# Performance work log

Measured on AMD Instinct MI355X. Metric: run time of the kernel, lower is better.

## Reference

```python
import jax, jax.numpy as jnp
import numpy as np

DIM = 192
NUM_HEADS = 6
WH, WW = 7, 7
N = WH * WW  # 49 tokens per window
C2 = 2 * DIM  # concatenated channel dim = 384
SCALE = (DIM // NUM_HEADS) ** -0.5  # module uses dim//num_heads, not C2//num_heads
NW = 64  # number of windows per image
B_ = 2048  # num_windows * batch


def _relative_position_index():
    ch = np.arange(WH)
    cw = np.arange(WW)
    coords = np.stack(np.meshgrid(ch, cw, indexing='ij')).reshape(2, -1)  # [2, N]
    rel = coords[:, :, None] - coords[:, None, :]  # [2, N, N]
    rel = rel.transpose(1, 2, 0).astype(np.int64)  # [N, N, 2]
    rel[..., 0] += WH - 1
    rel[..., 1] += WW - 1
    rel[..., 0] *= 2 * WW - 1
    return jnp.asarray(rel.sum(-1))  # [N, N]

REL_IDX = _relative_position_index()


def setup_inputs() -> dict:
    key = jax.random.key(0)
    ks = jax.random.split(key, 8)
    x = jax.random.normal(ks[0], (B_, N, DIM), dtype=jnp.float32)
    y = jax.random.normal(ks[1], (B_, N, DIM), dtype=jnp.float32)
    mask = jax.random.normal(ks[2], (NW, N, N), dtype=jnp.float32)
    w_qkv = jax.random.normal(ks[3], (6 * DIM, C2), dtype=jnp.float32) * 0.02
    b_qkv = jnp.zeros((6 * DIM,), dtype=jnp.float32)
    w_proj = jax.random.normal(ks[4], (DIM, C2), dtype=jnp.float32) * 0.02
    b_proj = jnp.zeros((DIM,), dtype=jnp.float32)
    bias_table = jax.random.normal(ks[5], ((2 * WH - 1) * (2 * WW - 1), NUM_HEADS), dtype=jnp.float32) * 0.02
    return {"x": x, "y": y, "mask": mask, "w_qkv": w_qkv, "b_qkv": b_qkv,
            "w_proj": w_proj, "b_proj": b_proj, "bias_table": bias_table}


def reference(x, y, mask, w_qkv, b_qkv, w_proj, b_proj, bias_table):
    Bc = x.shape[0]
    Dh = C2 // NUM_HEADS  # 64
    xy = jnp.concatenate([x, y], axis=2)  # [B_, N, 2*dim]
    qkv = xy @ w_qkv.T + b_qkv  # [B_, N, 6*dim]
    qkv = qkv.reshape(Bc, N, 3, NUM_HEADS, Dh).transpose(2, 0, 3, 1, 4)  # [3, B_, H, N, Dh]
    q, k, v = qkv[0] * SCALE, qkv[1], qkv[2]
    attn = jnp.einsum('bhnd,bhmd->bhnm', q, k)  # [B_, H, N, N]
    rpb = bias_table[REL_IDX]  # [N, N, H]
    attn = attn + rpb.transpose(2, 0, 1)[None]
    nW = mask.shape[0]
    attn = attn.reshape(Bc // nW, nW, NUM_HEADS, N, N) + mask[None, :, None]
    attn = attn.reshape(Bc, NUM_HEADS, N, N)
    attn = jax.nn.softmax(attn, axis=-1)
    out = jnp.einsum('bhnm,bhmd->bhnd', attn, v)  # [B_, H, N, Dh]
    out = out.transpose(0, 2, 1, 3).reshape(Bc, N, C2)
    return out @ w_proj.T + b_proj  # [B_, N, dim]
```

## Files before the change

kernel.cpp:

```cpp
#include <hip/hip_runtime.h>
#include <hip/hip_bf16.h>


typedef __attribute__((ext_vector_type(8))) short short8;
typedef __attribute__((ext_vector_type(4))) float f32x4;

#define SCALE 0.17677669529663687f

#define WQF_OFF    0ul
#define WQF_BYTES  (864ul*1024)
#define WPF_OFF    (WQF_OFF + WQF_BYTES)
#define WPF_BYTES  (144ul*1024)
#define COMB_OFF   (WPF_OFF + WPF_BYTES)
#define COMB_BYTES (64ul*6*4096*4)
#define XYF_OFF    (COMB_OFF + COMB_BYTES)
#define XYF_BYTES  (2048ul*48*1024)
#define OF_OFF     (XYF_OFF + XYF_BYTES)
#define OF_BYTES   XYF_BYTES
#define WS_NEED    (OF_OFF + OF_BYTES)

__device__ __forceinline__ unsigned short f2bf(float f){
  unsigned u = __builtin_bit_cast(unsigned, f);
  u = u + 0x7fffu + ((u >> 16) & 1u);
  return (unsigned short)(u >> 16);
}
__device__ __forceinline__ unsigned long long pack4(float4 v){
  return (unsigned long long)f2bf(v.x) | ((unsigned long long)f2bf(v.y) << 16)
       | ((unsigned long long)f2bf(v.z) << 32) | ((unsigned long long)f2bf(v.w) << 48);
}

__global__ void k0_wfrag(const float* __restrict__ wq_f, const float* __restrict__ wp_f,
                         unsigned short* __restrict__ wqf, unsigned short* __restrict__ wpf){
  int t = blockIdx.x*256 + threadIdx.x;
  int fragidx = t >> 6, l = t & 63;
  const float* src; unsigned short* dst;
  if (fragidx < 864){
    int h = fragidx/144, rem = fragidx - h*144;
    int ct = rem/12, kt = rem - ct*12;
    int row = (ct>>2)*384 + h*64 + (ct&3)*16 + (l&15);
    src = wq_f + (long)row*384 + kt*32 + (l>>4)*8;
    dst = wqf + (long)fragidx*512 + l*8;
  } else {
    int fid = fragidx - 864;
    int ct = fid/12, kt = fid - ct*12;
    int row = ct*16 + (l&15);
    src = wp_f + (long)row*384 + kt*32 + (l>>4)*8;
    dst = wpf + (long)fid*512 + l*8;
  }
  short8 v;
  #pragma unroll
  for (int e = 0; e < 8; ++e) v[e] = (short)f2bf(src[e]);
  *(short8*)dst = v;
}

__global__ void prep_comb(const float* __restrict__ mask, const float* __restrict__ btab,
                          float* __restrict__ comb){
  int idx = blockIdx.x * 256 + threadIdx.x;
  int j = idx & 63, i = (idx >> 6) & 63, rest = idx >> 12;
  int h = rest % 6, w = rest / 6;
  float v;
  if (i < 49 && j < 49){
    int di = i / 7 - j / 7 + 6;
    int dj = i % 7 - j % 7 + 6;
    v = btab[(di * 13 + dj) * 6 + h] + mask[(w * 49 + i) * 49 + j];
  } else {
    v = (j >= 49) ? -1e30f : 0.0f;
  }
  comb[idx] = v;
}

__global__ void k1_xyfrag(const float* __restrict__ x, const float* __restrict__ y,
                          unsigned short* __restrict__ xyf){
  const int kt  = blockIdx.x;
  const int win = blockIdx.y;
  const int mt  = threadIdx.x >> 6;
  const int l   = threadIdx.x & 63;
  const int row = mt*16 + (l & 15);
  const int c0  = kt*32 + (l >> 4)*8;
  short8 v = {};
  if (row < 49){
    const float* src = (kt < 6) ? (x + ((long)win*49 + row)*192 + c0)
                                : (y + ((long)win*49 + row)*192 + (c0 - 192));
    float4 f0 = *(const float4*)src, f1 = *(const float4*)(src+4);
    unsigned long long lo = pack4(f0), hi = pack4(f1);
    #pragma unroll
    for (int e = 0; e < 4; ++e){ v[e] = (short)(lo >> (16*e)); v[4+e] = (short)(hi >> (16*e)); }
  }
  *(short8*)(xyf + (((long)win*12 + kt)*4 + mt)*512 + l*8) = v;
}

__device__ __forceinline__ int swz(int r, int b){ return b ^ ((r & 7) << 4); }
__device__ __forceinline__ int a_q (int r, int c){ return 0     + swz(r, r*128 + c*2); }
__device__ __forceinline__ int a_k (int r, int c){ return 8192  + swz(r, r*128 + c*2); }
__device__ __forceinline__ int a_vt(int r, int c){ return 16384 + swz(r, r*128 + c*2); }

__global__ __launch_bounds__(256, 4)
void k2_qkv_attn(const unsigned short* __restrict__ xyf, const unsigned short* __restrict__ wqf,
                 const float* __restrict__ bqkv, const float* __restrict__ comb,
                 unsigned short* __restrict__ Of){
  __shared__ __align__(16) unsigned char smem[24576];
  const int h = blockIdx.x, win = blockIdx.y;
  const int tid = threadIdx.x, w = tid>>6, l = tid&63, l15 = l&15, lg = l>>4;

  float bias[3];
  #pragma unroll
  for (int nt = 0; nt < 3; ++nt){
    int n = w*48 + nt*16 + l15;
    bias[nt] = bqkv[(n>>6)*384 + h*64 + (n&63)];
  }

  f32x4 acc[4][3] = {};
  const unsigned short* Ab = xyf + (long)win*24576;
  const unsigned short* Bb = wqf + ((long)h*12 + w*3)*12*512;
  short8 aA[2][4], bB[2][3];
  #pragma unroll
  for (int mt = 0; mt < 4; ++mt) aA[0][mt] = *(const short8*)(Ab + mt*512 + l*8);
  #pragma unroll
  for (int nt = 0; nt < 3; ++nt) bB[0][nt] = *(const short8*)(Bb + (nt*12)*512 + l*8);
  #pragma unroll
  for (int kt = 0; kt < 12; ++kt){
    const int cur = kt & 1, nxt = cur ^ 1;
    if (kt < 11){
      #pragma unroll
      for (int mt = 0; mt < 4; ++mt)
        aA[nxt][mt] = *(const short8*)(Ab + ((kt+1)*4 + mt)*512 + l*8);
      #pragma unroll
      for (int nt = 0; nt < 3; ++nt)
        bB[nxt][nt] = *(const short8*)(Bb + (nt*12 + kt+1)*512 + l*8);
    }
    #pragma unroll
    for (int nt = 0; nt < 3; ++nt){
      #pragma unroll
      for (int mt = 0; mt < 4; ++mt)
        acc[mt][nt] = __builtin_amdgcn_mfma_f32_16x16x32_bf16(aA[cur][mt], bB[cur][nt], acc[mt][nt], 0, 0, 0);
    }
  }

  const float* cb = comb + ((long)((win & 63)*6 + h))*4096 + (w*16 + l15)*64 + lg*4;
  float4 cbv[4];
  #pragma unroll
  for (int nt = 0; nt < 4; ++nt) cbv[nt] = *(const float4*)(cb + nt*16);

  #pragma unroll
  for (int nt = 0; nt < 3; ++nt){
    int ct = w*3 + nt, s = ct >> 2, d16 = (ct & 3) * 16;
    if (s == 2){
      #pragma unroll
      for (int mt = 0; mt < 4; ++mt){
        float4 vv;
        vv.x = acc[mt][nt][0] + bias[nt]; vv.y = acc[mt][nt][1] + bias[nt];
        vv.z = acc[mt][nt][2] + bias[nt]; vv.w = acc[mt][nt][3] + bias[nt];
        *(unsigned long long*)(smem + a_vt(d16 + l15, mt*16 + lg*4)) = pack4(vv);
      }
    } else {
      float sc = (s == 0) ? SCALE : 1.0f;
      #pragma unroll
      for (int mt = 0; mt < 4; ++mt){
        #pragma unroll
        for (int j = 0; j < 4; ++j){
          int row = mt*16 + lg*4 + j;
          float v = (acc[mt][nt][j] + bias[nt]) * sc;
          int addr = (s == 0) ? a_q(row, d16 + l15) : a_k(row, d16 + l15);
          *(unsigned short*)(smem + addr) = f2bf(v);
        }
      }
    }
  }
  __syncthreads();

  short8 bq[2];
  #pragma unroll
  for (int ks = 0; ks < 2; ++ks)
    bq[ks] = *(const short8*)(smem + a_q(w*16 + l15, ks*32 + lg*8));
  f32x4 st[4] = {};
  #pragma unroll
  for (int ks = 0; ks < 2; ++ks){
    #pragma unroll
    for (int nt = 0; nt < 4; ++nt){
      short8 ak = *(const short8*)(smem + a_k(nt*16 + l15, ks*32 + lg*8));
      st[nt] = __builtin_amdgcn_mfma_f32_16x16x32_bf16(ak, bq[ks], st[nt], 0, 0, 0);
    }
  }
  #pragma unroll
  for (int nt = 0; nt < 4; ++nt){
    st[nt][0] += cbv[nt].x; st[nt][1] += cbv[nt].y;
    st[nt][2] += cbv[nt].z; st[nt][3] += cbv[nt].w;
  }
  float mx;
  {
    float m0 = fmaxf(fmaxf(st[0][0], st[0][1]), fmaxf(st[0][2], st[0][3]));
    float m1 = fmaxf(fmaxf(st[1][0], st[1][1]), fmaxf(st[1][2], st[1][3]));
    float m2 = fmaxf(fmaxf(st[2][0], st[2][1]), fmaxf(st[2][2], st[2][3]));
    float m3 = fmaxf(fmaxf(st[3][0], st[3][1]), fmaxf(st[3][2], st[3][3]));
    mx = fmaxf(fmaxf(m0, m1), fmaxf(m2, m3));
  }
  mx = fmaxf(mx, __shfl_xor(mx, 16));
  mx = fmaxf(mx, __shfl_xor(mx, 32));
  float ssum = 0.f;
  #pragma unroll
  for (int nt = 0; nt < 4; ++nt){
    #pragma unroll
    for (int j = 0; j < 4; ++j){
      float e = __expf(st[nt][j] - mx);
      st[nt][j] = e; ssum += e;
    }
  }
  ssum += __shfl_xor(ssum, 16);
  ssum += __shfl_xor(ssum, 32);
  const float inv = 1.0f / ssum;

  #pragma unroll
  for (int nt = 0; nt < 4; ++nt){
    float4 vv;
    vv.x = st[nt][0]*inv; vv.y = st[nt][1]*inv; vv.z = st[nt][2]*inv; vv.w = st[nt][3]*inv;
    *(unsigned long long*)(smem + a_q(w*16 + l15, nt*16 + lg*4)) = pack4(vv);
  }

  short8 ap[2];
  #pragma unroll
  for (int ks = 0; ks < 2; ++ks)
    ap[ks] = *(const short8*)(smem + a_q(w*16 + l15, ks*32 + lg*8));
  f32x4 oacc[4] = {};
  #pragma unroll
  for (int ks = 0; ks < 2; ++ks){
    #pragma unroll
    for (int nt = 0; nt < 4; ++nt){
      short8 bv = *(const short8*)(smem + a_vt(nt*16 + l15, ks*32 + lg*8));
      oacc[nt] = __builtin_amdgcn_mfma_f32_16x16x32_bf16(ap[ks], bv, oacc[nt], 0, 0, 0);
    }
  }
  #pragma unroll
  for (int nt = 0; nt < 4; ++nt){
    #pragma unroll
    for (int j = 0; j < 4; ++j)
      *(unsigned short*)(smem + a_q(w*16 + lg*4 + j, nt*16 + l15)) = f2bf(oacc[nt][j]);
  }
  unsigned short* Ob = Of + (((long)win*12 + h*2)*4 + w)*512 + l*8;
  #pragma unroll
  for (int ks = 0; ks < 2; ++ks){
    short8 o8 = *(const short8*)(smem + a_q(w*16 + l15, ks*32 + lg*8));
    *(short8*)(Ob + ks*4*512) = o8;
  }
}

__global__ __launch_bounds__(256, 4)
void k3_proj(const unsigned short* __restrict__ Of, const unsigned short* __restrict__ wpf,
             const float* __restrict__ bproj, float* __restrict__ out){
  const int win = blockIdx.x;
  const int tid = threadIdx.x, w = tid>>6, l = tid&63, l15 = l&15, lg = l>>4;
  float bp[3]; int np[3];
  #pragma unroll
  for (int nt = 0; nt < 3; ++nt){
    np[nt] = w*48 + nt*16 + l15;
    bp[nt] = bproj[np[nt]];
  }
  f32x4 acc[4][3] = {};
  const unsigned short* Ab = Of + (long)win*24576;
  const unsigned short* Bb = wpf + (long)(w*3)*12*512;
  short8 aA[2][4], bB[2][3];
  #pragma unroll
  for (int mt = 0; mt < 4; ++mt) aA[0][mt] = *(const short8*)(Ab + mt*512 + l*8);
  #pragma unroll
  for (int nt = 0; nt < 3; ++nt) bB[0][nt] = *(const short8*)(Bb + (nt*12)*512 + l*8);
  #pragma unroll
  for (int kt = 0; kt < 12; ++kt){
    const int cur = kt & 1, nxt = cur ^ 1;
    if (kt < 11){
      #pragma unroll
      for (int mt = 0; mt < 4; ++mt)
        aA[nxt][mt] = *(const short8*)(Ab + ((kt+1)*4 + mt)*512 + l*8);
      #pragma unroll
      for (int nt = 0; nt < 3; ++nt)
        bB[nxt][nt] = *(const short8*)(Bb + (nt*12 + kt+1)*512 + l*8);
    }
    #pragma unroll
    for (int nt = 0; nt < 3; ++nt){
      #pragma unroll
      for (int mt = 0; mt < 4; ++mt)
        acc[mt][nt] = __builtin_amdgcn_mfma_f32_16x16x32_bf16(aA[cur][mt], bB[cur][nt], acc[mt][nt], 0, 0, 0);
    }
  }
  #pragma unroll
  for (int mt = 0; mt < 4; ++mt){
    #pragma unroll
    for (int j = 0; j < 4; ++j){
      int row = mt*16 + lg*4 + j;
      if (row < 49){
        float* o = out + ((long)win*49 + row)*192;
        #pragma unroll
        for (int nt = 0; nt < 3; ++nt)
          o[np[nt]] = acc[mt][nt][j] + bp[nt];
      }
    }
  }
}

#define FB_WQ_ELEMS (1152*384)
#define FB_WP_ELEMS (192*384)
#define FB_WP_OFF   (FB_WQ_ELEMS*2)
#define FB_COMB_OFF (FB_WP_OFF + FB_WP_ELEMS*2)

__global__ void prep_weights_fb(const float* __restrict__ wq_f, const float* __restrict__ wp_f,
                                unsigned short* __restrict__ wq, unsigned short* __restrict__ wp){
  int gid = blockIdx.x * 256 + threadIdx.x;
  if (gid < FB_WQ_ELEMS) wq[gid] = f2bf(wq_f[gid]);
  else { int g = gid - FB_WQ_ELEMS; if (g < FB_WP_ELEMS) wp[g] = f2bf(wp_f[g]); }
}
__device__ __forceinline__ int fb_xy(int r, int c){ return 0      + swz(r, r*768 + c*2); }
__device__ __forceinline__ int fb_q (int r, int c){ return 49152  + swz(r, r*128 + c*2); }
__device__ __forceinline__ int fb_k (int r, int c){ return 57344  + swz(r, r*128 + c*2); }
__device__ __forceinline__ int fb_vt(int r, int c){ return 65536  + swz(r, r*128 + c*2); }
__device__ __forceinline__ int fb_p (int r, int c){ return 73728  + swz(r, r*128 + c*2); }

__global__ __launch_bounds__(256, 2)
void fused_attn_fb(const float* __restrict__ x, const float* __restrict__ y,
                   const float* __restrict__ bqkv, const float* __restrict__ bproj,
                   const unsigned short* __restrict__ wq, const unsigned short* __restrict__ wp,
                   const float* __restrict__ comb, float* __restrict__ out){
  __shared__ __align__(16) unsigned char smem[81920];
  const int b = blockIdx.x, tid = threadIdx.x;
  const int w = tid>>6, l = tid&63, l15 = l&15, lg = l>>4;
  {
    const float4* x4 = (const float4*)x + b * 2352;
    const float4* y4 = (const float4*)y + b * 2352;
    for (int idx = tid; idx < 2352; idx += 256){
      int r = idx / 48, c4 = (idx % 48) * 4;
      float4 vx = x4[idx], vy = y4[idx];
      *(unsigned long long*)(smem + fb_xy(r, c4))       = pack4(vx);
      *(unsigned long long*)(smem + fb_xy(r, 192 + c4)) = pack4(vy);
    }
    for (int idx = tid; idx < 1440; idx += 256){
      int r = 49 + idx / 96, c4 = (idx % 96) * 4;
      *(unsigned long long*)(smem + fb_xy(r, c4)) = 0ull;
    }
  }
  __syncthreads();
  const float* cbB = comb + (long)(b & 63) * (6 * 4096);
  f32x4 pacc[4][3] = {};
  int np[3]; float bp[3];
  #pragma unroll
  for (int nt = 0; nt < 3; ++nt){ np[nt] = w*48 + nt*16 + l15; bp[nt] = bproj[np[nt]]; }
  #pragma unroll 1
  for (int h = 0; h < 6; ++h){
    f32x4 acc[4][3] = {};
    int wrow[3]; float bias[3];
    #pragma unroll
    for (int nt = 0; nt < 3; ++nt){
      int n = np[nt];
      wrow[nt] = (n >> 6) * 384 + h * 64 + (n & 63);
      bias[nt] = bqkv[wrow[nt]];
    }
    #pragma unroll 4
    for (int kt = 0; kt < 12; ++kt){
      int k0 = kt * 32;
      short8 a[4];
      #pragma unroll
      for (int mt = 0; mt < 4; ++mt)
        a[mt] = *(const short8*)(smem + fb_xy(mt*16 + l15, k0 + lg*8));
      #pragma unroll
      for (int nt = 0; nt < 3; ++nt){
        short8 bb = *(const short8*)(wq + (long)wrow[nt]*384 + k0 + lg*8);
        #pragma unroll
        for (int mt = 0; mt < 4; ++mt)
          acc[mt][nt] = __builtin_amdgcn_mfma_f32_16x16x32_bf16(a[mt], bb, acc[mt][nt], 0, 0, 0);
      }
    }
    #pragma unroll
    for (int nt = 0; nt < 3; ++nt){
      int n = np[nt], s = n >> 6, d = n & 63;
      #pragma unroll
      for (int mt = 0; mt < 4; ++mt){
        #pragma unroll
        for (int j = 0; j < 4; ++j){
          int row = mt*16 + lg*4 + j;
          float v = acc[mt][nt][j] + bias[nt];
          if (s == 0) v *= SCALE;
          int addr = (s==0) ? fb_q(row,d) : (s==1) ? fb_k(row,d) : fb_vt(d,row);
          *(unsigned short*)(smem + addr) = f2bf(v);
        }
      }
    }
    __syncthreads();
    short8 aq[2];
    #pragma unroll
    for (int ks = 0; ks < 2; ++ks)
      aq[ks] = *(const short8*)(smem + fb_q(w*16 + l15, ks*32 + lg*8));
    f32x4 sacc[4] = {};
    #pragma unroll
    for (int ks = 0; ks < 2; ++ks)
      #pragma unroll
      for (int nt = 0; nt < 4; ++nt){
        short8 bk = *(const short8*)(smem + fb_k(nt*16 + l15, ks*32 + lg*8));
        sacc[nt] = __builtin_amdgcn_mfma_f32_16x16x32_bf16(aq[ks], bk, sacc[nt], 0, 0, 0);
      }
    const float* cb = cbB + h * 4096;
    float rs[4];
    #pragma unroll
    for (int j = 0; j < 4; ++j){
      int r = w*16 + lg*4 + j;
      #pragma unroll
      for (int nt = 0; nt < 4; ++nt) sacc[nt][j] += cb[r*64 + nt*16 + l15];
      float m = fmaxf(fmaxf(sacc[0][j], sacc[1][j]), fmaxf(sacc[2][j], sacc[3][j]));
      #pragma unroll
      for (int dlt = 1; dlt < 16; dlt <<= 1) m = fmaxf(m, __shfl_xor(m, dlt));
      float ssum = 0.f;
      #pragma unroll
      for (int nt = 0; nt < 4; ++nt){
        float e = __expf(sacc[nt][j] - m);
        sacc[nt][j] = e; ssum += e;
      }
      #pragma unroll
      for (int dlt = 1; dlt < 16; dlt <<= 1) ssum += __shfl_xor(ssum, dlt);
      rs[j] = ssum;
      #pragma unroll
      for (int nt = 0; nt < 4; ++nt)
        *(unsigned short*)(smem + fb_p(r, nt*16 + l15)) = f2bf(sacc[nt][j]);
    }
    short8 ap[2];
    #pragma unroll
    for (int ks = 0; ks < 2; ++ks)
      ap[ks] = *(const short8*)(smem + fb_p(w*16 + l15, ks*32 + lg*8));
    f32x4 oacc[4] = {};
    #pragma unroll
    for (int ks = 0; ks < 2; ++ks)
      #pragma unroll
      for (int nt = 0; nt < 4; ++nt){
        short8 bv = *(const short8*)(smem + fb_vt(nt*16 + l15, ks*32 + lg*8));
        oacc[nt] = __builtin_amdgcn_mfma_f32_16x16x32_bf16(ap[ks], bv, oacc[nt], 0, 0, 0);
      }
    float inv[4];
    #pragma unroll
    for (int j = 0; j < 4; ++j) inv[j] = 1.0f / rs[j];
    #pragma unroll
    for (int nt = 0; nt < 4; ++nt)
      #pragma unroll
      for (int j = 0; j < 4; ++j){
        int row = w*16 + lg*4 + j;
        *(unsigned short*)(smem + fb_p(row, nt*16 + l15)) = f2bf(oacc[nt][j] * inv[j]);
      }
    __syncthreads();
    #pragma unroll
    for (int ks = 0; ks < 2; ++ks){
      short8 ao8[4];
      #pragma unroll
      for (int mt = 0; mt < 4; ++mt)
        ao8[mt] = *(const short8*)(smem + fb_p(mt*16 + l15, ks*32 + lg*8));
      #pragma unroll
      for (int nt = 0; nt < 3; ++nt){
        short8 bb = *(const short8*)(wp + (long)np[nt]*384 + h*64 + ks*32 + lg*8);
        #pragma unroll
        for (int mt = 0; mt < 4; ++mt)
          pacc[mt][nt] = __builtin_amdgcn_mfma_f32_16x16x32_bf16(ao8[mt], bb, pacc[mt][nt], 0, 0, 0);
      }
    }
  }
  #pragma unroll
  for (int mt = 0; mt < 4; ++mt)
    #pragma unroll
    for (int j = 0; j < 4; ++j){
      int row = mt*16 + lg*4 + j;
      if (row < 49){
        float* o = out + ((long)b*49 + row)*192;
        #pragma unroll
        for (int nt = 0; nt < 3; ++nt)
          o[np[nt]] = pacc[mt][nt][j] + bp[nt];
      }
    }
}

extern "C" void kernel_launch(void* const* d_in, const int* in_sizes, int n_in,
                              void* d_out, int out_size, void* d_ws, size_t ws_size,
                              hipStream_t stream){
  (void)in_sizes; (void)n_in; (void)out_size;
  const float* x     = (const float*)d_in[0];
  const float* y     = (const float*)d_in[1];
  const float* mask  = (const float*)d_in[2];
  const float* wq_f  = (const float*)d_in[3];
  const float* bqkv  = (const float*)d_in[4];
  const float* wp_f  = (const float*)d_in[5];
  const float* bproj = (const float*)d_in[6];
  const float* btab  = (const float*)d_in[7];
  float* out = (float*)d_out;

  if (ws_size >= WS_NEED){
    unsigned short* wqf = (unsigned short*)((char*)d_ws + WQF_OFF);
    unsigned short* wpf = (unsigned short*)((char*)d_ws + WPF_OFF);
    float*          cmb = (float*)((char*)d_ws + COMB_OFF);
    unsigned short* xyf = (unsigned short*)((char*)d_ws + XYF_OFF);
    unsigned short* Ofr = (unsigned short*)((char*)d_ws + OF_OFF);
    hipLaunchKernelGGL(k0_wfrag,    dim3(252),     dim3(256), 0, stream, wq_f, wp_f, wqf, wpf);
    hipLaunchKernelGGL(prep_comb,   dim3(6144),    dim3(256), 0, stream, mask, btab, cmb);
    hipLaunchKernelGGL(k1_xyfrag,   dim3(12,2048), dim3(256), 0, stream, x, y, xyf);
    hipLaunchKernelGGL(k2_qkv_attn, dim3(6,2048),  dim3(256), 0, stream, xyf, wqf, bqkv, cmb, Ofr);
    hipLaunchKernelGGL(k3_proj,     dim3(2048),    dim3(256), 0, stream, Ofr, wpf, bproj, out);
  } else {
    unsigned short* wq  = (unsigned short*)d_ws;
    unsigned short* wp  = (unsigned short*)((char*)d_ws + FB_WP_OFF);
    float*          cmb = (float*)((char*)d_ws + FB_COMB_OFF);
    hipLaunchKernelGGL(prep_weights_fb, dim3(2016), dim3(256), 0, stream, wq_f, wp_f, wq, wp);
    hipLaunchKernelGGL(prep_comb,       dim3(6144), dim3(256), 0, stream, mask, btab, cmb);
    hipLaunchKernelGGL(fused_attn_fb,   dim3(2048), dim3(256), 0, stream,
                       x, y, bqkv, bproj, wq, wp, cmb, out);
  }
}
```

Baseline: 269.0 us.

## Stage activation tiles into LDS via global_load_lds and fold scale/bias into weights

In the QKV-attention and projection kernels, the activation tile for each window is now loaded once into shared memory with direct global-to-LDS async loads. Before, each wave reloaded the whole tile redundantly from global memory, and those loads are now served from LDS. The q scale is folded into the pre-converted bf16 weights and the bias, and accumulators start from the bias, which removes the epilogue add and multiply. Shared memory per block grows from 24 KB to 48 KB, which can reduce occupancy, and scaling before bf16 rounding slightly changes numerics.

```diff
diff --git a/kernel.cpp b/kernel.cpp
--- a/kernel.cpp
+++ b/kernel.cpp
@@ -29,17 +29,25 @@
        | ((unsigned long long)f2bf(v.z) << 32) | ((unsigned long long)f2bf(v.w) << 48);
 }
 
+__device__ __forceinline__ void gll16(const void* g, void* l){
+  __builtin_amdgcn_global_load_lds(
+      (const __attribute__((address_space(1))) unsigned int*)g,
+      (__attribute__((address_space(3))) unsigned int*)l, 16, 0, 0);
+}
+
 __global__ void k0_wfrag(const float* __restrict__ wq_f, const float* __restrict__ wp_f,
                          unsigned short* __restrict__ wqf, unsigned short* __restrict__ wpf){
   int t = blockIdx.x*256 + threadIdx.x;
   int fragidx = t >> 6, l = t & 63;
   const float* src; unsigned short* dst;
+  float sc = 1.0f;
   if (fragidx < 864){
     int h = fragidx/144, rem = fragidx - h*144;
     int ct = rem/12, kt = rem - ct*12;
     int row = (ct>>2)*384 + h*64 + (ct&3)*16 + (l&15);
     src = wq_f + (long)row*384 + kt*32 + (l>>4)*8;
     dst = wqf + (long)fragidx*512 + l*8;
+    if (ct < 4) sc = SCALE;
   } else {
     int fid = fragidx - 864;
     int ct = fid/12, kt = fid - ct*12;
@@ -49,7 +57,7 @@
   }
   short8 v;
   #pragma unroll
-  for (int e = 0; e < 8; ++e) v[e] = (short)f2bf(src[e]);
+  for (int e = 0; e < 8; ++e) v[e] = (short)f2bf(src[e] * sc);
   *(short8*)dst = v;
 }
 
@@ -98,48 +106,64 @@
 void k2_qkv_attn(const unsigned short* __restrict__ xyf, const unsigned short* __restrict__ wqf,
                  const float* __restrict__ bqkv, const float* __restrict__ comb,
                  unsigned short* __restrict__ Of){
-  __shared__ __align__(16) unsigned char smem[24576];
+  __shared__ __align__(16) unsigned char smem[49152];
   const int h = blockIdx.x, win = blockIdx.y;
   const int tid = threadIdx.x, w = tid>>6, l = tid&63, l15 = l&15, lg = l>>4;
 
+  {
+    const char*    gs = (const char*)(xyf + (long)win*24576) + w*12288 + l*16;
+    unsigned char* ls = smem + w*12288;
+    #pragma unroll
+    for (int i = 0; i < 12; ++i)
+      gll16(gs + i*1024, ls + i*1024);
+  }
+
+  const float* cb = comb + ((long)((win & 63)*6 + h))*4096 + (w*16 + l15)*64 + lg*4;
+  float4 cbv[4];
+  #pragma unroll
+  for (int nt = 0; nt < 4; ++nt) cbv[nt] = *(const float4*)(cb + nt*16);
   float bias[3];
   #pragma unroll
   for (int nt = 0; nt < 3; ++nt){
-    int n = w*48 + nt*16 + l15;
-    bias[nt] = bqkv[(n>>6)*384 + h*64 + (n&63)];
-  }
-
-  f32x4 acc[4][3] = {};
-  const unsigned short* Ab = xyf + (long)win*24576;
+    int ct = w*3 + nt, s = ct >> 2;
+    bias[nt] = bqkv[s*384 + h*64 + (ct & 3)*16 + l15];
+    if (s == 0) bias[nt] *= SCALE;
+  }
+
   const unsigned short* Bb = wqf + ((long)h*12 + w*3)*12*512;
-  short8 aA[2][4], bB[2][3];
-  #pragma unroll
-  for (int mt = 0; mt < 4; ++mt) aA[0][mt] = *(const short8*)(Ab + mt*512 + l*8);
+  short8 bB[2][3];
   #pragma unroll
   for (int nt = 0; nt < 3; ++nt) bB[0][nt] = *(const short8*)(Bb + (nt*12)*512 + l*8);
+  f32x4 acc[4][3];
+  #pragma unroll
+  for (int mt = 0; mt < 4; ++mt)
+    #pragma unroll
+    for (int nt = 0; nt < 3; ++nt)
+      #pragma unroll
+      for (int j = 0; j < 4; ++j) acc[mt][nt][j] = bias[nt];
+
+  __syncthreads();
+
   #pragma unroll
   for (int kt = 0; kt < 12; ++kt){
     const int cur = kt & 1, nxt = cur ^ 1;
     if (kt < 11){
       #pragma unroll
-      for (int mt = 0; mt < 4; ++mt)
-        aA[nxt][mt] = *(const short8*)(Ab + ((kt+1)*4 + mt)*512 + l*8);
-      #pragma unroll
       for (int nt = 0; nt < 3; ++nt)
         bB[nxt][nt] = *(const short8*)(Bb + (nt*12 + kt+1)*512 + l*8);
     }
+    short8 aA[4];
+    #pragma unroll
+    for (int mt = 0; mt < 4; ++mt)
+      aA[mt] = *(const short8*)(smem + (kt*4 + mt)*1024 + l*16);
     #pragma unroll
     for (int nt = 0; nt < 3; ++nt){
       #pragma unroll
       for (int mt = 0; mt < 4; ++mt)
-        acc[mt][nt] = __builtin_amdgcn_mfma_f32_16x16x32_bf16(aA[cur][mt], bB[cur][nt], acc[mt][nt], 0, 0, 0);
-    }
-  }
-
-  const float* cb = comb + ((long)((win & 63)*6 + h))*4096 + (w*16 + l15)*64 + lg*4;
-  float4 cbv[4];
-  #pragma unroll
-  for (int nt = 0; nt < 4; ++nt) cbv[nt] = *(const float4*)(cb + nt*16);
+        acc[mt][nt] = __builtin_amdgcn_mfma_f32_16x16x32_bf16(aA[mt], bB[cur][nt], acc[mt][nt], 0, 0, 0);
+    }
+  }
+  __syncthreads();
 
   #pragma unroll
   for (int nt = 0; nt < 3; ++nt){
@@ -148,20 +172,18 @@
       #pragma unroll
       for (int mt = 0; mt < 4; ++mt){
         float4 vv;
-        vv.x = acc[mt][nt][0] + bias[nt]; vv.y = acc[mt][nt][1] + bias[nt];
-        vv.z = acc[mt][nt][2] + bias[nt]; vv.w = acc[mt][nt][3] + bias[nt];
+        vv.x = acc[mt][nt][0]; vv.y = acc[mt][nt][1];
+        vv.z = acc[mt][nt][2]; vv.w = acc[mt][nt][3];
         *(unsigned long long*)(smem + a_vt(d16 + l15, mt*16 + lg*4)) = pack4(vv);
       }
     } else {
-      float sc = (s == 0) ? SCALE : 1.0f;
       #pragma unroll
       for (int mt = 0; mt < 4; ++mt){
         #pragma unroll
         for (int j = 0; j < 4; ++j){
           int row = mt*16 + lg*4 + j;
-          float v = (acc[mt][nt][j] + bias[nt]) * sc;
           int addr = (s == 0) ? a_q(row, d16 + l15) : a_k(row, d16 + l15);
-          *(unsigned short*)(smem + addr) = f2bf(v);
+          *(unsigned short*)(smem + addr) = f2bf(acc[mt][nt][j]);
         }
       }
     }
@@ -246,38 +268,53 @@
 __global__ __launch_bounds__(256, 4)
 void k3_proj(const unsigned short* __restrict__ Of, const unsigned short* __restrict__ wpf,
              const float* __restrict__ bproj, float* __restrict__ out){
+  __shared__ __align__(16) unsigned char smem[49152];
   const int win = blockIdx.x;
   const int tid = threadIdx.x, w = tid>>6, l = tid&63, l15 = l&15, lg = l>>4;
+  {
+    const char*    gs = (const char*)(Of + (long)win*24576) + w*12288 + l*16;
+    unsigned char* ls = smem + w*12288;
+    #pragma unroll
+    for (int i = 0; i < 12; ++i)
+      gll16(gs + i*1024, ls + i*1024);
+  }
   float bp[3]; int np[3];
   #pragma unroll
   for (int nt = 0; nt < 3; ++nt){
     np[nt] = w*48 + nt*16 + l15;
     bp[nt] = bproj[np[nt]];
   }
-  f32x4 acc[4][3] = {};
-  const unsigned short* Ab = Of + (long)win*24576;
   const unsigned short* Bb = wpf + (long)(w*3)*12*512;
-  short8 aA[2][4], bB[2][3];
-  #pragma unroll
-  for (int mt = 0; mt < 4; ++mt) aA[0][mt] = *(const short8*)(Ab + mt*512 + l*8);
+  short8 bB[2][3];
   #pragma unroll
   for (int nt = 0; nt < 3; ++nt) bB[0][nt] = *(const short8*)(Bb + (nt*12)*512 + l*8);
+  f32x4 acc[4][3];
+  #pragma unroll
+  for (int mt = 0; mt < 4; ++mt)
+    #pragma unroll
+    for (int nt = 0; nt < 3; ++nt)
+      #pragma unroll
+      for (int j = 0; j < 4; ++j) acc[mt][nt][j] = bp[nt];
+
+  __syncthreads();
+
   #pragma unroll
   for (int kt = 0; kt < 12; ++kt){
     const int cur = kt & 1, nxt = cur ^ 1;
     if (kt < 11){
       #pragma unroll
-      for (int mt = 0; mt < 4; ++mt)
-        aA[nxt][mt] = *(const short8*)(Ab + ((kt+1)*4 + mt)*512 + l*8);
-      #pragma unroll
       for (int nt = 0; nt < 3; ++nt)
         bB[nxt][nt] = *(const short8*)(Bb + (nt*12 + kt+1)*512 + l*8);
     }
+    short8 aA[4];
+    #pragma unroll
+    for (int mt = 0; mt < 4; ++mt)
+      aA[mt] = *(const short8*)(smem + (kt*4 + mt)*1024 + l*16);
     #pragma unroll
     for (int nt = 0; nt < 3; ++nt){
       #pragma unroll
       for (int mt = 0; mt < 4; ++mt)
-        acc[mt][nt] = __builtin_amdgcn_mfma_f32_16x16x32_bf16(aA[cur][mt], bB[cur][nt], acc[mt][nt], 0, 0, 0);
+        acc[mt][nt] = __builtin_amdgcn_mfma_f32_16x16x32_bf16(aA[mt], bB[cur][nt], acc[mt][nt], 0, 0, 0);
     }
   }
   #pragma unroll
@@ -289,7 +326,7 @@
         float* o = out + ((long)win*49 + row)*192;
         #pragma unroll
         for (int nt = 0; nt < 3; ++nt)
-          o[np[nt]] = acc[mt][nt][j] + bp[nt];
+          o[np[nt]] = acc[mt][nt][j];
       }
     }
   }
```

New measurement: 302.1 us. 1.12x slower.
